# Optimization experiments

Measured on AMD Instinct MI355X. Metric: run time of the kernel, lower is better.

The kernel has to match this reference:

```python
import jax, jax.numpy as jnp
import numpy as np

EPS = 1e-12
REF = jnp.array([0.0, 0.0, 1.0], dtype=jnp.float32)  # reference direction


def _l2_normalize(x, axis=-1):
    n = jnp.linalg.norm(x, axis=axis, keepdims=True)
    return x / jnp.maximum(n, EPS)


def _rotate_ref_by_quat(q):
    # q: (B, 4) as (w, x, y, z); rotates REF=[0,0,1]:
    # v' = v + 2w (q_v x v) + 2 q_v x (q_v x v)
    w = q[:, 0:1]           # (B, 1)
    qv = q[:, 1:4]          # (B, 3)
    cross1 = jnp.cross(qv, REF[None, :])  # (B, 3)
    cross2 = jnp.cross(qv, cross1)        # (B, 3)
    return REF[None, :] + 2.0 * w * cross1 + 2.0 * cross2


def setup_inputs() -> dict:
    key = jax.random.key(0)
    k1, k2 = jax.random.split(key)
    B = 8388608
    pred = jax.random.normal(k1, (B, 4), dtype=jnp.float32)
    target = jax.random.normal(k2, (B, 4), dtype=jnp.float32)
    return {"pred": pred, "target": target}


def reference(pred, target):
    pred_q = _l2_normalize(pred, axis=1)
    target_q = _l2_normalize(target, axis=1)
    pred_v = _l2_normalize(_rotate_ref_by_quat(pred_q), axis=1)
    target_v = _l2_normalize(_rotate_ref_by_quat(target_q), axis=1)
    cos_sim = jnp.clip(jnp.sum(pred_v * target_v, axis=1), -1.0, 1.0)  # (B,)
    angle = jnp.arccos(cos_sim)
    return jnp.mean(angle * angle)  # reduction='mean'
```

## Files before the change

### kernel.cpp

```cpp
#include <hip/hip_runtime.h>
#include <math.h>

#define NBLK 2048
#define NTHR 256

__global__ __launch_bounds__(NTHR) void drl_main(
    const float4* __restrict__ pred,
    const float4* __restrict__ targ,
    float* __restrict__ partial,
    int B)
{
    const int tid = blockIdx.x * blockDim.x + threadIdx.x;
    const int stride = gridDim.x * blockDim.x;
    float acc = 0.0f;
    for (int i = tid; i < B; i += stride) {
        float4 p = pred[i];
        float4 t = targ[i];
        float n2p = p.x*p.x + p.y*p.y + p.z*p.z + p.w*p.w;
        float ip = 1.0f / fmaxf(sqrtf(n2p), 1e-12f);
        float pw = p.x*ip, px = p.y*ip, py = p.z*ip, pz = p.w*ip;
        float n2t = t.x*t.x + t.y*t.y + t.z*t.z + t.w*t.w;
        float it = 1.0f / fmaxf(sqrtf(n2t), 1e-12f);
        float tw = t.x*it, tx = t.y*it, ty = t.z*it, tz = t.w*it;
        float pvx = 2.0f*(pw*py + px*pz);
        float pvy = 2.0f*(py*pz - pw*px);
        float pvz = 1.0f - 2.0f*(px*px + py*py);
        float tvx = 2.0f*(tw*ty + tx*tz);
        float tvy = 2.0f*(ty*tz - tw*tx);
        float tvz = 1.0f - 2.0f*(tx*tx + ty*ty);
        float inp = 1.0f / fmaxf(sqrtf(pvx*pvx + pvy*pvy + pvz*pvz), 1e-12f);
        float inv = 1.0f / fmaxf(sqrtf(tvx*tvx + tvy*tvy + tvz*tvz), 1e-12f);
        float c = (pvx*tvx + pvy*tvy + pvz*tvz) * inp * inv;
        c = fminf(1.0f, fmaxf(-1.0f, c));
        float a = acosf(c);
        acc += a * a;
    }
    #pragma unroll
    for (int off = 32; off > 0; off >>= 1)
        acc += __shfl_down(acc, off, 64);
    __shared__ float smem[NTHR / 64];
    const int lane = threadIdx.x & 63;
    const int wid  = threadIdx.x >> 6;
    if (lane == 0) smem[wid] = acc;
    __syncthreads();
    if (threadIdx.x == 0) {
        float s = 0.0f;
        #pragma unroll
        for (int w = 0; w < NTHR / 64; ++w) s += smem[w];
        partial[blockIdx.x] = s;
    }
}

__global__ __launch_bounds__(NTHR) void drl_finalize(
    const float* __restrict__ partial, float* __restrict__ out, int n, float invB)
{
    float acc = 0.0f;
    for (int i = threadIdx.x; i < n; i += blockDim.x) acc += partial[i];
    #pragma unroll
    for (int off = 32; off > 0; off >>= 1)
        acc += __shfl_down(acc, off, 64);
    __shared__ float smem[NTHR / 64];
    const int lane = threadIdx.x & 63;
    const int wid  = threadIdx.x >> 6;
    if (lane == 0) smem[wid] = acc;
    __syncthreads();
    if (threadIdx.x == 0) {
        float s = 0.0f;
        #pragma unroll
        for (int w = 0; w < NTHR / 64; ++w) s += smem[w];
        out[0] = s * invB;
    }
}

extern "C" void kernel_launch(void* const* d_in, const int* in_sizes, int n_in,
                              void* d_out, int out_size, void* d_ws, size_t ws_size,
                              hipStream_t stream) {
    const float4* pred = (const float4*)d_in[0];
    const float4* targ = (const float4*)d_in[1];
    float* out = (float*)d_out;
    float* partial = (float*)d_ws;
    const int B = in_sizes[0] / 4;
    drl_main<<<NBLK, NTHR, 0, stream>>>(pred, targ, partial, B);
    drl_finalize<<<1, NTHR, 0, stream>>>(partial, out, NBLK, 1.0f / (float)B);
}
```

Measured before the change: 55.04 us.

## Fuse finalize into main kernel via last-block ticket and simplify per-row math

Replaces the two-kernel reduction with a single kernel in which the last block to finish, found through an atomic ticket counter, sums the partials. The per-row math skips quaternion normalization by using homogeneous rotated vectors, merges the two vector norms into one rsqrt, and swaps acosf for a polynomial approximation. The grid-stride loop is unrolled by two so each thread has more loads in flight. The single kernel adds a memset launch to reset the counter, and the acos polynomial introduces small approximation error.

```diff
diff --git a/kernel.cpp b/kernel.cpp
--- a/kernel.cpp
+++ b/kernel.cpp
@@ -4,71 +4,86 @@
 #define NBLK 2048
 #define NTHR 256
 
-__global__ __launch_bounds__(NTHR) void drl_main(
+__device__ __forceinline__ float row_angle2(float4 p, float4 t) {
+    float n2p = p.x*p.x + p.y*p.y + p.z*p.z + p.w*p.w;
+    float upx = 2.0f*(p.x*p.z + p.y*p.w);
+    float upy = 2.0f*(p.z*p.w - p.x*p.y);
+    float upz = n2p - 2.0f*(p.y*p.y + p.z*p.z);
+
+    float n2t = t.x*t.x + t.y*t.y + t.z*t.z + t.w*t.w;
+    float utx = 2.0f*(t.x*t.z + t.y*t.w);
+    float uty = 2.0f*(t.z*t.w - t.x*t.y);
+    float utz = n2t - 2.0f*(t.y*t.y + t.z*t.z);
+
+    float d   = upx*utx + upy*uty + upz*utz;
+    float mp  = upx*upx + upy*upy + upz*upz;
+    float mt  = utx*utx + uty*uty + utz*utz;
+    float m   = fmaxf(mp*mt, 1e-24f);
+    float c   = d * rsqrtf(m);
+    c = fminf(1.0f, fmaxf(-1.0f, c));
+
+    float a = fabsf(c);
+    float r = sqrtf(1.0f - a) *
+              (1.5707288f + a*(-0.2121144f + a*(0.0742610f + a*(-0.0187293f))));
+    float ang = (c >= 0.0f) ? r : 3.14159265358979f - r;
+    return ang * ang;
+}
+
+__global__ __launch_bounds__(NTHR) void drl_fused(
     const float4* __restrict__ pred,
     const float4* __restrict__ targ,
     float* __restrict__ partial,
-    int B)
+    int*  __restrict__ counter,
+    float* __restrict__ out,
+    int B, float invB)
 {
-    const int tid = blockIdx.x * blockDim.x + threadIdx.x;
     const int stride = gridDim.x * blockDim.x;
     float acc = 0.0f;
-    for (int i = tid; i < B; i += stride) {
-        float4 p = pred[i];
-        float4 t = targ[i];
-        float n2p = p.x*p.x + p.y*p.y + p.z*p.z + p.w*p.w;
-        float ip = 1.0f / fmaxf(sqrtf(n2p), 1e-12f);
-        float pw = p.x*ip, px = p.y*ip, py = p.z*ip, pz = p.w*ip;
-        float n2t = t.x*t.x + t.y*t.y + t.z*t.z + t.w*t.w;
-        float it = 1.0f / fmaxf(sqrtf(n2t), 1e-12f);
-        float tw = t.x*it, tx = t.y*it, ty = t.z*it, tz = t.w*it;
-        float pvx = 2.0f*(pw*py + px*pz);
-        float pvy = 2.0f*(py*pz - pw*px);
-        float pvz = 1.0f - 2.0f*(px*px + py*py);
-        float tvx = 2.0f*(tw*ty + tx*tz);
-        float tvy = 2.0f*(ty*tz - tw*tx);
-        float tvz = 1.0f - 2.0f*(tx*tx + ty*ty);
-        float inp = 1.0f / fmaxf(sqrtf(pvx*pvx + pvy*pvy + pvz*pvz), 1e-12f);
-        float inv = 1.0f / fmaxf(sqrtf(tvx*tvx + tvy*tvy + tvz*tvz), 1e-12f);
-        float c = (pvx*tvx + pvy*tvy + pvz*tvz) * inp * inv;
-        c = fminf(1.0f, fmaxf(-1.0f, c));
-        float a = acosf(c);
-        acc += a * a;
+    int i = blockIdx.x * blockDim.x + threadIdx.x;
+    for (; i + stride < B; i += 2*stride) {
+        float4 p0 = pred[i],        t0 = targ[i];
+        float4 p1 = pred[i+stride], t1 = targ[i+stride];
+        acc += row_angle2(p0, t0);
+        acc += row_angle2(p1, t1);
     }
+    if (i < B) acc += row_angle2(pred[i], targ[i]);
+
     #pragma unroll
     for (int off = 32; off > 0; off >>= 1)
         acc += __shfl_down(acc, off, 64);
     __shared__ float smem[NTHR / 64];
+    __shared__ int lastFlag;
     const int lane = threadIdx.x & 63;
     const int wid  = threadIdx.x >> 6;
     if (lane == 0) smem[wid] = acc;
     __syncthreads();
     if (threadIdx.x == 0) {
+        float bsum = 0.0f;
+        #pragma unroll
+        for (int w = 0; w < NTHR / 64; ++w) bsum += smem[w];
+        __hip_atomic_store(&partial[blockIdx.x], bsum,
+                           __ATOMIC_RELEASE, __HIP_MEMORY_SCOPE_AGENT);
+        int ticket = __hip_atomic_fetch_add(counter, 1,
+                           __ATOMIC_ACQ_REL, __HIP_MEMORY_SCOPE_AGENT);
+        lastFlag = (ticket == (int)gridDim.x - 1) ? 1 : 0;
+    }
+    __syncthreads();
+    if (lastFlag) {
         float s = 0.0f;
+        for (int j = threadIdx.x; j < (int)gridDim.x; j += NTHR)
+            s += __hip_atomic_load(&partial[j],
+                     __ATOMIC_RELAXED, __HIP_MEMORY_SCOPE_AGENT);
         #pragma unroll
-        for (int w = 0; w < NTHR / 64; ++w) s += smem[w];
-        partial[blockIdx.x] = s;
-    }
-}
-
-__global__ __launch_bounds__(NTHR) void drl_finalize(
-    const float* __restrict__ partial, float* __restrict__ out, int n, float invB)
-{
-    float acc = 0.0f;
-    for (int i = threadIdx.x; i < n; i += blockDim.x) acc += partial[i];
-    #pragma unroll
-    for (int off = 32; off > 0; off >>= 1)
-        acc += __shfl_down(acc, off, 64);
-    __shared__ float smem[NTHR / 64];
-    const int lane = threadIdx.x & 63;
-    const int wid  = threadIdx.x >> 6;
-    if (lane == 0) smem[wid] = acc;
-    __syncthreads();
-    if (threadIdx.x == 0) {
-        float s = 0.0f;
-        #pragma unroll
-        for (int w = 0; w < NTHR / 64; ++w) s += smem[w];
-        out[0] = s * invB;
+        for (int off = 32; off > 0; off >>= 1)
+            s += __shfl_down(s, off, 64);
+        if (lane == 0) smem[wid] = s;
+        __syncthreads();
+        if (threadIdx.x == 0) {
+            float tot = 0.0f;
+            #pragma unroll
+            for (int w = 0; w < NTHR / 64; ++w) tot += smem[w];
+            out[0] = tot * invB;
+        }
     }
 }
 
@@ -79,7 +94,9 @@
     const float4* targ = (const float4*)d_in[1];
     float* out = (float*)d_out;
     float* partial = (float*)d_ws;
+    int* counter   = (int*)((char*)d_ws + NBLK * sizeof(float));
     const int B = in_sizes[0] / 4;
-    drl_main<<<NBLK, NTHR, 0, stream>>>(pred, targ, partial, B);
-    drl_finalize<<<1, NTHR, 0, stream>>>(partial, out, NBLK, 1.0f / (float)B);
+    hipMemsetAsync(counter, 0, sizeof(int), stream);
+    drl_fused<<<NBLK, NTHR, 0, stream>>>(pred, targ, partial, counter, out,
+                                         B, 1.0f / (float)B);
 }
```

New measurement: 165.9 us. +201.4%, slower.
